# Optimization experiments

Measured on AMD Instinct MI355X. Metric: run time of the kernel, lower is better.

Reference implementation:

```python
import jax, jax.numpy as jnp
import numpy as np

B, T, D = 8, 128, 256


def setup_inputs() -> dict:
    key = jax.random.key(0)
    k1, k2 = jax.random.split(key)
    dec_t = jax.random.normal(k1, (B, D), dtype=jnp.float32)
    enc_out = jax.random.normal(k2, (B, T, D), dtype=jnp.float32)
    return {"dec_t": dec_t, "enc_out": enc_out}


def reference(dec_t, enc_out):
    # Faithful vectorization of the original double Python loop.
    # Per timestep t: E[b,p,q] = exp(dec_t[b,p] * enc_out[b,t,q])  (outer product)
    # a_ts[b,p,q] = E[b,p,q] / rowsum[b,q]   (torch broadcast [D,D]/[D] divides
    #               each column q by the row-sum of row q: rowsum[q]=sum_r E[q,r])
    # contribution to c_t: a_ts[b,p,q] * enc_out[b,t,q], accumulated over t,
    # then summed over p.
    # => c_t[b,q] = sum_t enc_out[b,t,q] * colsum[b,t,q] / rowsum[b,t,q]
    E = jnp.exp(dec_t[:, None, :, None] * enc_out[:, :, None, :])  # [B,T,D,D]
    colsum = E.sum(axis=2)  # sum over p -> [B,T,D] indexed by q
    rowsum = E.sum(axis=3)  # sum over r -> [B,T,D] indexed by q (row q of outer)
    return jnp.sum(enc_out * colsum / rowsum, axis=1)  # [B,D]
```

## Files before the change

### kernel.cpp

```cpp
#include <hip/hip_runtime.h>

#define BB 8
#define TT 128
#define DD 256
#define BT (BB * TT)
#define LOG2E 1.44269504088896340736f

__device__ __forceinline__ float exp2_fast(float z) {
    const float r = __builtin_rintf(z);
    const float f = z - r;
    float p = 1.5252733804059840e-5f;
    p = __builtin_fmaf(p, f, 1.5403530393381609e-4f);
    p = __builtin_fmaf(p, f, 1.3333558146428443e-3f);
    p = __builtin_fmaf(p, f, 9.6181291076284772e-3f);
    p = __builtin_fmaf(p, f, 5.5504108664821580e-2f);
    p = __builtin_fmaf(p, f, 2.4022650695910072e-1f);
    p = __builtin_fmaf(p, f, 6.9314718055994531e-1f);
    p = __builtin_fmaf(p, f, 1.0f);
    return ldexpf(p, (int)r);
}

__global__ __launch_bounds__(256, 4) void attn_sym_kernel(
    const float* __restrict__ dec,
    const float* __restrict__ enc,
    float* __restrict__ ws) {
    const int blk = blockIdx.x;
    const int b = blk >> 7;
    const int tid = threadIdx.x;

    const float* __restrict__ drow = dec + b * DD;
    const float* __restrict__ erow = enc + blk * DD;

    const float dv = drow[tid];
    const float ev = erow[tid];
    const float dl2 = dv * LOG2E;
    const float el2 = ev * LOG2E;

    float cs0 = 0.f, cs1 = 0.f, cs2 = 0.f, cs3 = 0.f;
    float rs0 = 0.f, rs1 = 0.f, rs2 = 0.f, rs3 = 0.f;
    #pragma unroll 4
    for (int k = 0; k < DD; k += 4) {
        float4 d4 = *reinterpret_cast<const float4*>(drow + k);
        float4 e4 = *reinterpret_cast<const float4*>(erow + k);
        cs0 += __builtin_amdgcn_exp2f(d4.x * el2);
        cs1 += __builtin_amdgcn_exp2f(d4.y * el2);
        cs2 += __builtin_amdgcn_exp2f(d4.z * el2);
        cs3 += __builtin_amdgcn_exp2f(d4.w * el2);
        rs0 += exp2_fast(dl2 * e4.x);
        rs1 += exp2_fast(dl2 * e4.y);
        rs2 += exp2_fast(dl2 * e4.z);
        rs3 += exp2_fast(dl2 * e4.w);
    }
    const float cs = (cs0 + cs1) + (cs2 + cs3);
    const float rs = (rs0 + rs1) + (rs2 + rs3);

    ws[blk * DD + tid] = ev * cs / rs;
}

__global__ __launch_bounds__(256) void reduce_t_kernel(
    const float* __restrict__ ws, float* __restrict__ out) {
    __shared__ float red[8][32];
    const int b = blockIdx.x >> 3;
    const int qc = blockIdx.x & 7;
    const int qlane = threadIdx.x & 31;
    const int tc = threadIdx.x >> 5;
    const int q = qc * 32 + qlane;

    const float* p = ws + (b * TT + tc * 16) * DD + q;
    float a0 = 0.f, a1 = 0.f, a2 = 0.f, a3 = 0.f;
    #pragma unroll
    for (int t = 0; t < 16; t += 4) {
        a0 += p[(t + 0) * DD];
        a1 += p[(t + 1) * DD];
        a2 += p[(t + 2) * DD];
        a3 += p[(t + 3) * DD];
    }
    red[tc][qlane] = (a0 + a1) + (a2 + a3);
    __syncthreads();
    if (tc == 0) {
        float s = 0.f;
        #pragma unroll
        for (int u = 0; u < 8; ++u) s += red[u][qlane];
        out[b * DD + q] = s;
    }
}

extern "C" void kernel_launch(void* const* d_in, const int* in_sizes, int n_in,
                              void* d_out, int out_size, void* d_ws, size_t ws_size,
                              hipStream_t stream) {
    const float* dec = (const float*)d_in[0];
    const float* enc = (const float*)d_in[1];
    float* out = (float*)d_out;
    float* ws = (float*)d_ws;

    attn_sym_kernel<<<BT, 256, 0, stream>>>(dec, enc, ws);
    reduce_t_kernel<<<BB * 8, 256, 0, stream>>>(ws, out);
}
```

Baseline: 82.02 us.

## Split row/col exp sums across two half-blocks and use hardware exp2

Replaces the software polynomial exp2 for row sums with the hardware exp2 instruction, removing a long chain of FMAs per element. Splits each (b,t) block's reduction over D into two halves handled by separate blocks, writing partial col/row sums to workspace. The final ratio and multiplication by enc move into the reduction kernel. This adds workspace traffic and a heavier reduce pass, and slightly reduces accuracy of the row-sum exponentials.

```diff
diff --git a/kernel.cpp b/kernel.cpp
--- a/kernel.cpp
+++ b/kernel.cpp
@@ -4,34 +4,24 @@
 #define TT 128
 #define DD 256
 #define BT (BB * TT)
+#define SZ (BT * DD)
 #define LOG2E 1.44269504088896340736f
 
-__device__ __forceinline__ float exp2_fast(float z) {
-    const float r = __builtin_rintf(z);
-    const float f = z - r;
-    float p = 1.5252733804059840e-5f;
-    p = __builtin_fmaf(p, f, 1.5403530393381609e-4f);
-    p = __builtin_fmaf(p, f, 1.3333558146428443e-3f);
-    p = __builtin_fmaf(p, f, 9.6181291076284772e-3f);
-    p = __builtin_fmaf(p, f, 5.5504108664821580e-2f);
-    p = __builtin_fmaf(p, f, 2.4022650695910072e-1f);
-    p = __builtin_fmaf(p, f, 6.9314718055994531e-1f);
-    p = __builtin_fmaf(p, f, 1.0f);
-    return ldexpf(p, (int)r);
-}
-
-__global__ __launch_bounds__(256, 4) void attn_sym_kernel(
+__global__ __launch_bounds__(256, 8) void attn_half_kernel(
     const float* __restrict__ dec,
     const float* __restrict__ enc,
     float* __restrict__ ws) {
-    const int blk = blockIdx.x;
-    const int b = blk >> 7;
+    const int blk = blockIdx.x >> 1;
+    const int h   = blockIdx.x & 1;
+    const int b   = blk >> 7;
     const int tid = threadIdx.x;
 
-    const float* __restrict__ drow = dec + b * DD;
-    const float* __restrict__ erow = enc + blk * DD;
+    const float* __restrict__ dbase = dec + b * DD;
+    const float* __restrict__ erow  = enc + blk * DD;
+    const float* __restrict__ drh   = dbase + h * 128;
+    const float* __restrict__ erh   = erow + h * 128;
 
-    const float dv = drow[tid];
+    const float dv = dbase[tid];
     const float ev = erow[tid];
     const float dl2 = dv * LOG2E;
     const float el2 = ev * LOG2E;
@@ -39,26 +29,26 @@
     float cs0 = 0.f, cs1 = 0.f, cs2 = 0.f, cs3 = 0.f;
     float rs0 = 0.f, rs1 = 0.f, rs2 = 0.f, rs3 = 0.f;
     #pragma unroll 4
-    for (int k = 0; k < DD; k += 4) {
-        float4 d4 = *reinterpret_cast<const float4*>(drow + k);
-        float4 e4 = *reinterpret_cast<const float4*>(erow + k);
+    for (int k = 0; k < 128; k += 4) {
+        float4 d4 = *reinterpret_cast<const float4*>(drh + k);
+        float4 e4 = *reinterpret_cast<const float4*>(erh + k);
         cs0 += __builtin_amdgcn_exp2f(d4.x * el2);
         cs1 += __builtin_amdgcn_exp2f(d4.y * el2);
         cs2 += __builtin_amdgcn_exp2f(d4.z * el2);
         cs3 += __builtin_amdgcn_exp2f(d4.w * el2);
-        rs0 += exp2_fast(dl2 * e4.x);
-        rs1 += exp2_fast(dl2 * e4.y);
-        rs2 += exp2_fast(dl2 * e4.z);
-        rs3 += exp2_fast(dl2 * e4.w);
+        rs0 += __builtin_amdgcn_exp2f(dl2 * e4.x);
+        rs1 += __builtin_amdgcn_exp2f(dl2 * e4.y);
+        rs2 += __builtin_amdgcn_exp2f(dl2 * e4.z);
+        rs3 += __builtin_amdgcn_exp2f(dl2 * e4.w);
     }
-    const float cs = (cs0 + cs1) + (cs2 + cs3);
-    const float rs = (rs0 + rs1) + (rs2 + rs3);
-
-    ws[blk * DD + tid] = ev * cs / rs;
+    const int o = blk * DD + tid;
+    ws[h * SZ + o]       = (cs0 + cs1) + (cs2 + cs3);
+    ws[(2 + h) * SZ + o] = (rs0 + rs1) + (rs2 + rs3);
 }
 
 __global__ __launch_bounds__(256) void reduce_t_kernel(
-    const float* __restrict__ ws, float* __restrict__ out) {
+    const float* __restrict__ ws, const float* __restrict__ enc,
+    float* __restrict__ out) {
     __shared__ float red[8][32];
     const int b = blockIdx.x >> 3;
     const int qc = blockIdx.x & 7;
@@ -66,14 +56,18 @@
     const int tc = threadIdx.x >> 5;
     const int q = qc * 32 + qlane;
 
-    const float* p = ws + (b * TT + tc * 16) * DD + q;
+    const int base = (b * TT + tc * 16) * DD + q;
     float a0 = 0.f, a1 = 0.f, a2 = 0.f, a3 = 0.f;
     #pragma unroll
     for (int t = 0; t < 16; t += 4) {
-        a0 += p[(t + 0) * DD];
-        a1 += p[(t + 1) * DD];
-        a2 += p[(t + 2) * DD];
-        a3 += p[(t + 3) * DD];
+        const int i0 = base + (t + 0) * DD;
+        const int i1 = base + (t + 1) * DD;
+        const int i2 = base + (t + 2) * DD;
+        const int i3 = base + (t + 3) * DD;
+        a0 += enc[i0] * (ws[i0] + ws[SZ + i0]) / (ws[2 * SZ + i0] + ws[3 * SZ + i0]);
+        a1 += enc[i1] * (ws[i1] + ws[SZ + i1]) / (ws[2 * SZ + i1] + ws[3 * SZ + i1]);
+        a2 += enc[i2] * (ws[i2] + ws[SZ + i2]) / (ws[2 * SZ + i2] + ws[3 * SZ + i2]);
+        a3 += enc[i3] * (ws[i3] + ws[SZ + i3]) / (ws[2 * SZ + i3] + ws[3 * SZ + i3]);
     }
     red[tc][qlane] = (a0 + a1) + (a2 + a3);
     __syncthreads();
@@ -93,6 +87,6 @@
     float* out = (float*)d_out;
     float* ws = (float*)d_ws;
 
-    attn_sym_kernel<<<BT, 256, 0, stream>>>(dec, enc, ws);
-    reduce_t_kernel<<<BB * 8, 256, 0, stream>>>(ws, out);
+    attn_half_kernel<<<BT * 2, 256, 0, stream>>>(dec, enc, ws);
+    reduce_t_kernel<<<BB * 8, 256, 0, stream>>>(ws, enc, out);
 }
```

Result: faster. 71.99 us (-12.2%).

## Compute exp outer-product once and derive row sums via LDS transpose

Applied to the files above, without the earlier changes.

Each block computes the exp outer-product only once: each thread's column sums come from the hardware exp2, and the same values are written into a padded shared-memory stripe. Row sums are then read back transposed from shared memory and accumulated with LDS atomics. This removes the second, software-polynomial exponential pass that previously produced row sums. In exchange it adds about 33KB of shared memory per block, two barriers per stripe, and misaligned float4 LDS reads caused by the 257-element row pitch.

```diff
diff --git a/kernel.cpp b/kernel.cpp
--- a/kernel.cpp
+++ b/kernel.cpp
@@ -4,23 +4,12 @@
 #define TT 128
 #define DD 256
 #define BT (BB * TT)
+#define SP 32
+#define NS (DD / SP)
+#define RS 257
 #define LOG2E 1.44269504088896340736f
 
-__device__ __forceinline__ float exp2_fast(float z) {
-    const float r = __builtin_rintf(z);
-    const float f = z - r;
-    float p = 1.5252733804059840e-5f;
-    p = __builtin_fmaf(p, f, 1.5403530393381609e-4f);
-    p = __builtin_fmaf(p, f, 1.3333558146428443e-3f);
-    p = __builtin_fmaf(p, f, 9.6181291076284772e-3f);
-    p = __builtin_fmaf(p, f, 5.5504108664821580e-2f);
-    p = __builtin_fmaf(p, f, 2.4022650695910072e-1f);
-    p = __builtin_fmaf(p, f, 6.9314718055994531e-1f);
-    p = __builtin_fmaf(p, f, 1.0f);
-    return ldexpf(p, (int)r);
-}
-
-__global__ __launch_bounds__(256, 4) void attn_sym_kernel(
+__global__ __launch_bounds__(256, 4) void attn_monce_kernel(
     const float* __restrict__ dec,
     const float* __restrict__ enc,
     float* __restrict__ ws) {
@@ -31,29 +20,48 @@
     const float* __restrict__ drow = dec + b * DD;
     const float* __restrict__ erow = enc + blk * DD;
 
-    const float dv = drow[tid];
+    __shared__ float m[SP * RS];
+    __shared__ float rowacc[DD];
+
     const float ev = erow[tid];
-    const float dl2 = dv * LOG2E;
     const float el2 = ev * LOG2E;
 
+    rowacc[tid] = 0.f;
+
+    const int rr = tid & 31;
+    const int cc = tid >> 5;
+    float* mwr = m + tid;
+    const float* mrd = m + rr * RS + cc * 32;
+
     float cs0 = 0.f, cs1 = 0.f, cs2 = 0.f, cs3 = 0.f;
-    float rs0 = 0.f, rs1 = 0.f, rs2 = 0.f, rs3 = 0.f;
-    #pragma unroll 4
-    for (int k = 0; k < DD; k += 4) {
-        float4 d4 = *reinterpret_cast<const float4*>(drow + k);
-        float4 e4 = *reinterpret_cast<const float4*>(erow + k);
-        cs0 += __builtin_amdgcn_exp2f(d4.x * el2);
-        cs1 += __builtin_amdgcn_exp2f(d4.y * el2);
-        cs2 += __builtin_amdgcn_exp2f(d4.z * el2);
-        cs3 += __builtin_amdgcn_exp2f(d4.w * el2);
-        rs0 += exp2_fast(dl2 * e4.x);
-        rs1 += exp2_fast(dl2 * e4.y);
-        rs2 += exp2_fast(dl2 * e4.z);
-        rs3 += exp2_fast(dl2 * e4.w);
+    for (int s = 0; s < NS; ++s) {
+        const float* dstripe = drow + s * SP;
+        #pragma unroll
+        for (int p4 = 0; p4 < SP; p4 += 4) {
+            float4 d4 = *reinterpret_cast<const float4*>(dstripe + p4);
+            const float v0 = __builtin_amdgcn_exp2f(d4.x * el2);
+            const float v1 = __builtin_amdgcn_exp2f(d4.y * el2);
+            const float v2 = __builtin_amdgcn_exp2f(d4.z * el2);
+            const float v3 = __builtin_amdgcn_exp2f(d4.w * el2);
+            cs0 += v0; cs1 += v1; cs2 += v2; cs3 += v3;
+            mwr[(p4 + 0) * RS] = v0;
+            mwr[(p4 + 1) * RS] = v1;
+            mwr[(p4 + 2) * RS] = v2;
+            mwr[(p4 + 3) * RS] = v3;
+        }
+        __syncthreads();
+        float a0 = 0.f, a1 = 0.f, a2 = 0.f, a3 = 0.f;
+        #pragma unroll
+        for (int i = 0; i < 32; i += 4) {
+            float4 v = *reinterpret_cast<const float4*>(mrd + i);
+            a0 += v.x; a1 += v.y; a2 += v.z; a3 += v.w;
+        }
+        atomicAdd(&rowacc[s * SP + rr], (a0 + a1) + (a2 + a3));
+        __syncthreads();
     }
+
     const float cs = (cs0 + cs1) + (cs2 + cs3);
-    const float rs = (rs0 + rs1) + (rs2 + rs3);
-
+    const float rs = rowacc[tid];
     ws[blk * DD + tid] = ev * cs / rs;
 }
 
@@ -93,6 +101,6 @@
     float* out = (float*)d_out;
     float* ws = (float*)d_ws;
 
-    attn_sym_kernel<<<BT, 256, 0, stream>>>(dec, enc, ws);
+    attn_monce_kernel<<<BT, 256, 0, stream>>>(dec, enc, ws);
     reduce_t_kernel<<<BB * 8, 256, 0, stream>>>(ws, out);
 }
```

Result: slower. 103.8 us (+26.5%).

## Split exp work across block pairs mixing hardware exp2 and polynomial exp2

Applied to the files above, without the earlier changes.

Each (b,t) row is now handled by two blocks. One computes the first 160 k-terms with the hardware exp2 instruction for both sums, and the other computes the remaining 96 terms with the FMA polynomial exp2 for both sums. Partial column and row sums go to four workspace planes, and the reduction kernel combines them, multiplies by enc and divides. The aim is to balance the transcendental unit and the FMA pipes across concurrent blocks. In exchange the workspace traffic grows about fourfold, the reduce kernel must also read enc, and occupancy hints are raised to 8 blocks.

```diff
diff --git a/kernel.cpp b/kernel.cpp
--- a/kernel.cpp
+++ b/kernel.cpp
@@ -4,6 +4,8 @@
 #define TT 128
 #define DD 256
 #define BT (BB * TT)
+#define SZ (BT * DD)
+#define K0 160
 #define LOG2E 1.44269504088896340736f
 
 __device__ __forceinline__ float exp2_fast(float z) {
@@ -20,13 +22,15 @@
     return ldexpf(p, (int)r);
 }
 
-__global__ __launch_bounds__(256, 4) void attn_sym_kernel(
+__global__ __launch_bounds__(256, 8) void attn_hybrid_kernel(
     const float* __restrict__ dec,
     const float* __restrict__ enc,
     float* __restrict__ ws) {
-    const int blk = blockIdx.x;
-    const int b = blk >> 7;
-    const int tid = threadIdx.x;
+    const int blk2 = blockIdx.x;
+    const int blk  = blk2 >> 1;
+    const int meth = blk2 & 1;
+    const int b    = blk >> 7;
+    const int tid  = threadIdx.x;
 
     const float* __restrict__ drow = dec + b * DD;
     const float* __restrict__ erow = enc + blk * DD;
@@ -38,27 +42,45 @@
 
     float cs0 = 0.f, cs1 = 0.f, cs2 = 0.f, cs3 = 0.f;
     float rs0 = 0.f, rs1 = 0.f, rs2 = 0.f, rs3 = 0.f;
-    #pragma unroll 4
-    for (int k = 0; k < DD; k += 4) {
-        float4 d4 = *reinterpret_cast<const float4*>(drow + k);
-        float4 e4 = *reinterpret_cast<const float4*>(erow + k);
-        cs0 += __builtin_amdgcn_exp2f(d4.x * el2);
-        cs1 += __builtin_amdgcn_exp2f(d4.y * el2);
-        cs2 += __builtin_amdgcn_exp2f(d4.z * el2);
-        cs3 += __builtin_amdgcn_exp2f(d4.w * el2);
-        rs0 += exp2_fast(dl2 * e4.x);
-        rs1 += exp2_fast(dl2 * e4.y);
-        rs2 += exp2_fast(dl2 * e4.z);
-        rs3 += exp2_fast(dl2 * e4.w);
+
+    if (meth == 0) {
+        #pragma unroll 4
+        for (int k = 0; k < K0; k += 4) {
+            float4 d4 = *reinterpret_cast<const float4*>(drow + k);
+            float4 e4 = *reinterpret_cast<const float4*>(erow + k);
+            cs0 += __builtin_amdgcn_exp2f(d4.x * el2);
+            cs1 += __builtin_amdgcn_exp2f(d4.y * el2);
+            cs2 += __builtin_amdgcn_exp2f(d4.z * el2);
+            cs3 += __builtin_amdgcn_exp2f(d4.w * el2);
+            rs0 += __builtin_amdgcn_exp2f(dl2 * e4.x);
+            rs1 += __builtin_amdgcn_exp2f(dl2 * e4.y);
+            rs2 += __builtin_amdgcn_exp2f(dl2 * e4.z);
+            rs3 += __builtin_amdgcn_exp2f(dl2 * e4.w);
+        }
+    } else {
+        #pragma unroll 4
+        for (int k = K0; k < DD; k += 4) {
+            float4 d4 = *reinterpret_cast<const float4*>(drow + k);
+            float4 e4 = *reinterpret_cast<const float4*>(erow + k);
+            cs0 += exp2_fast(d4.x * el2);
+            cs1 += exp2_fast(d4.y * el2);
+            cs2 += exp2_fast(d4.z * el2);
+            cs3 += exp2_fast(d4.w * el2);
+            rs0 += exp2_fast(dl2 * e4.x);
+            rs1 += exp2_fast(dl2 * e4.y);
+            rs2 += exp2_fast(dl2 * e4.z);
+            rs3 += exp2_fast(dl2 * e4.w);
+        }
     }
-    const float cs = (cs0 + cs1) + (cs2 + cs3);
-    const float rs = (rs0 + rs1) + (rs2 + rs3);
 
-    ws[blk * DD + tid] = ev * cs / rs;
+    const int o = blk * DD + tid;
+    ws[meth * SZ + o]       = (cs0 + cs1) + (cs2 + cs3);
+    ws[(2 + meth) * SZ + o] = (rs0 + rs1) + (rs2 + rs3);
 }
 
 __global__ __launch_bounds__(256) void reduce_t_kernel(
-    const float* __restrict__ ws, float* __restrict__ out) {
+    const float* __restrict__ ws, const float* __restrict__ enc,
+    float* __restrict__ out) {
     __shared__ float red[8][32];
     const int b = blockIdx.x >> 3;
     const int qc = blockIdx.x & 7;
@@ -66,14 +88,18 @@
     const int tc = threadIdx.x >> 5;
     const int q = qc * 32 + qlane;
 
-    const float* p = ws + (b * TT + tc * 16) * DD + q;
+    const int base = (b * TT + tc * 16) * DD + q;
     float a0 = 0.f, a1 = 0.f, a2 = 0.f, a3 = 0.f;
     #pragma unroll
     for (int t = 0; t < 16; t += 4) {
-        a0 += p[(t + 0) * DD];
-        a1 += p[(t + 1) * DD];
-        a2 += p[(t + 2) * DD];
-        a3 += p[(t + 3) * DD];
+        const int i0 = base + (t + 0) * DD;
+        const int i1 = base + (t + 1) * DD;
+        const int i2 = base + (t + 2) * DD;
+        const int i3 = base + (t + 3) * DD;
+        a0 += enc[i0] * (ws[i0] + ws[SZ + i0]) / (ws[2 * SZ + i0] + ws[3 * SZ + i0]);
+        a1 += enc[i1] * (ws[i1] + ws[SZ + i1]) / (ws[2 * SZ + i1] + ws[3 * SZ + i1]);
+        a2 += enc[i2] * (ws[i2] + ws[SZ + i2]) / (ws[2 * SZ + i2] + ws[3 * SZ + i2]);
+        a3 += enc[i3] * (ws[i3] + ws[SZ + i3]) / (ws[2 * SZ + i3] + ws[3 * SZ + i3]);
     }
     red[tc][qlane] = (a0 + a1) + (a2 + a3);
     __syncthreads();
@@ -93,6 +119,6 @@
     float* out = (float*)d_out;
     float* ws = (float*)d_ws;
 
-    attn_sym_kernel<<<BT, 256, 0, stream>>>(dec, enc, ws);
-    reduce_t_kernel<<<BB * 8, 256, 0, stream>>>(ws, out);
+    attn_hybrid_kernel<<<BT * 2, 256, 0, stream>>>(dec, enc, ws);
+    reduce_t_kernel<<<BB * 8, 256, 0, stream>>>(ws, enc, out);
 }
```

New measurement: 81.66 us. No clear change (-0.4%).
